# Kernel tuning notes

Measured on AMD Instinct MI355X. Metric: run time of the kernel, lower is better.

## Reference

```python
import jax, jax.numpy as jnp
import numpy as np

B, C, K, T = 8, 256, 64, 1000
NORM_EPS = 1e-12


def setup_inputs() -> dict:
    key = jax.random.key(0)
    k_x, k_codes, k_scales = jax.random.split(key, 3)
    init_val = 1.0 / (K * C) ** 0.5
    x = jax.random.normal(k_x, (B, C, T), dtype=jnp.float32)
    codes = jax.random.uniform(k_codes, (C, K), dtype=jnp.float32,
                               minval=-init_val, maxval=init_val)
    scales = jax.random.uniform(k_scales, (K,), dtype=jnp.float32,
                                minval=0.0, maxval=1.0)
    return {"x": x, "codes": codes, "scales": scales}


def l2_normalize(t, axis, eps=NORM_EPS):
    n = jnp.sqrt(jnp.sum(t * t, axis=axis, keepdims=True))
    n = jnp.maximum(n, eps)
    return t / n


def reference(x, codes, scales):
    # x: (B, C, T); codes: (C, K); scales: (K,)
    residual = x[:, :, None, :] - codes[None, :, :, None]      # (B, C, K, T)
    residual_l2sqr = jnp.sum(residual * residual, axis=1)      # (B, K, T)
    weights_tc = jax.nn.softmax(-scales[None, :, None] * residual_l2sqr, axis=1)  # softmax over codes K
    embeddings = jnp.einsum('bckt,bkt->bkc', residual, weights_tc) / x.shape[-1]  # (B, K, C)
    embeddings = l2_normalize(embeddings, axis=-1)
    return embeddings
```

## Files before the change

### kernel.cpp

```cpp
#include <hip/hip_runtime.h>

constexpr int Bn  = 8;
constexpr int Cn  = 256;
constexpr int Kn  = 64;
constexpr int Tn  = 1000;
constexpr int CH  = 32;
constexpr int NCH = 32;

__global__ __launch_bounds__(512) void lde_ab(
    const float* __restrict__ x,
    const float* __restrict__ codes,
    const float* __restrict__ scales,
    float* __restrict__ part,
    float* __restrict__ Sp)
{
    __shared__ float xs[Cn * 33];
    __shared__ float cds[Cn * 64];
    __shared__ float ws[Kn * 36];
    __shared__ float xsq[CH];
    __shared__ float cpw[8 * 64];
    __shared__ float spw[8 * 64];

    const int tid  = threadIdx.x;
    const int wave = tid >> 6;
    const int lane = tid & 63;
    const int b    = blockIdx.x >> 5;
    const int ch   = blockIdx.x & 31;
    const int t0   = ch * CH;

    {
        const float4* cg = (const float4*)codes;
        float4*       cd = (float4*)cds;
#pragma unroll
        for (int r = 0; r < 8; ++r) cd[r * 512 + tid] = cg[r * 512 + tid];
    }

    {
        const float* xb = x + (size_t)b * Cn * Tn;
#pragma unroll
        for (int r = 0; r < 4; ++r) {
            int idx = r * 512 + tid;
            int c = idx >> 3, q = idx & 7;
            int t = t0 + 4 * q;
            float4 v;
            if (t + 3 < Tn) {
                v = *(const float4*)(xb + c * Tn + t);
            } else {
                v.x = (t     < Tn) ? xb[c * Tn + t]     : 0.f;
                v.y = (t + 1 < Tn) ? xb[c * Tn + t + 1] : 0.f;
                v.z = (t + 2 < Tn) ? xb[c * Tn + t + 2] : 0.f;
                v.w = (t + 3 < Tn) ? xb[c * Tn + t + 3] : 0.f;
            }
            float* d = xs + c * 33 + 4 * q;
            d[0] = v.x; d[1] = v.y; d[2] = v.z; d[3] = v.w;
        }
    }
    __syncthreads();

    {
        float cs = 0.f;
#pragma unroll 8
        for (int j = 0; j < 32; ++j) {
            float v = cds[(wave * 32 + j) * 64 + lane];
            cs = fmaf(v, v, cs);
        }
        cpw[wave * 64 + lane] = cs;
    }

    {
        const int kp    = lane >> 5;
        const int t     = lane & 31;
        const int kbase = wave * 8 + kp * 4;
        float m0 = 0.f, m1 = 0.f, m2 = 0.f, m3 = 0.f, xa = 0.f;
#pragma unroll 4
        for (int c = 0; c < Cn; ++c) {
            float4 cv = *(const float4*)(cds + c * 64 + kbase);
            float  xv = xs[c * 33 + t];
            m0 = fmaf(cv.x, xv, m0);
            m1 = fmaf(cv.y, xv, m1);
            m2 = fmaf(cv.z, xv, m2);
            m3 = fmaf(cv.w, xv, m3);
            xa = fmaf(xv, xv, xa);
        }
        ws[(kbase + 0) * 36 + t] = m0;
        ws[(kbase + 1) * 36 + t] = m1;
        ws[(kbase + 2) * 36 + t] = m2;
        ws[(kbase + 3) * 36 + t] = m3;
        if (tid < 32) xsq[tid] = xa;
    }
    __syncthreads();

    {
        const float sc  = scales[lane];
        float csq = 0.f;
#pragma unroll
        for (int w = 0; w < 8; ++w) csq += cpw[w * 64 + lane];
        float sp = 0.f;
#pragma unroll
        for (int j = 0; j < 4; ++j) {
            int t = wave * 4 + j;
            float mkt   = ws[lane * 36 + t];
            float logit = -sc * (xsq[t] - 2.f * mkt + csq);
            float mx = logit;
#pragma unroll
            for (int off = 32; off >= 1; off >>= 1)
                mx = fmaxf(mx, __shfl_xor(mx, off, 64));
            float e = __expf(logit - mx);
            float s = e;
#pragma unroll
            for (int off = 32; off >= 1; off >>= 1)
                s += __shfl_xor(s, off, 64);
            float wv = e * __builtin_amdgcn_rcpf(s);
            if (t0 + t >= Tn) wv = 0.f;
            sp += wv;
            ws[lane * 36 + t] = wv;
        }
        spw[wave * 64 + lane] = sp;
    }
    __syncthreads();

    if (wave == 0) {
        float s8 = 0.f;
#pragma unroll
        for (int w = 0; w < 8; ++w) s8 += spw[w * 64 + lane];
        Sp[((size_t)b * Kn + lane) * NCH + ch] = s8;
    }

    {
        const int k0 = wave * 8;
        float acc[4][8];
#pragma unroll
        for (int cc = 0; cc < 4; ++cc)
#pragma unroll
            for (int kk = 0; kk < 8; ++kk) acc[cc][kk] = 0.f;

#pragma unroll 2
        for (int q = 0; q < 8; ++q) {
            float xv[4][4];
#pragma unroll
            for (int cc = 0; cc < 4; ++cc) {
                const float* xp = xs + (lane + 64 * cc) * 33 + 4 * q;
                xv[cc][0] = xp[0]; xv[cc][1] = xp[1];
                xv[cc][2] = xp[2]; xv[cc][3] = xp[3];
            }
#pragma unroll
            for (int kk = 0; kk < 8; ++kk) {
                float4 wq = *(const float4*)(ws + (k0 + kk) * 36 + 4 * q);
#pragma unroll
                for (int cc = 0; cc < 4; ++cc) {
                    float a = acc[cc][kk];
                    a = fmaf(xv[cc][0], wq.x, a);
                    a = fmaf(xv[cc][1], wq.y, a);
                    a = fmaf(xv[cc][2], wq.z, a);
                    a = fmaf(xv[cc][3], wq.w, a);
                    acc[cc][kk] = a;
                }
            }
        }

#pragma unroll
        for (int kk = 0; kk < 8; ++kk) {
            float* pb = part + (((size_t)b * Kn + k0 + kk) * NCH + ch) * Cn + lane;
#pragma unroll
            for (int cc = 0; cc < 4; ++cc)
                pb[64 * cc] = acc[cc][kk];
        }
    }
}

__global__ __launch_bounds__(256) void lde_finish(
    const float* __restrict__ part,
    const float* __restrict__ Sp,
    const float* __restrict__ codes,
    float* __restrict__ out)
{
    const int b    = blockIdx.x >> 6;
    const int k    = blockIdx.x & 63;
    const int tid  = threadIdx.x;
    const int lane = tid & 63;
    const int wave = tid >> 6;

    __shared__ float red[4];

    float s = Sp[((size_t)b * Kn + k) * NCH + (tid & 31)];
#pragma unroll
    for (int off = 16; off >= 1; off >>= 1) s += __shfl_xor(s, off, 64);

    const int c = tid;
    const float* pb = part + ((size_t)b * Kn + k) * NCH * Cn + c;
    float val = 0.f;
#pragma unroll
    for (int chk = 0; chk < NCH; ++chk) val += pb[chk * Cn];

    float e = (val - codes[c * Kn + k] * s) * (1.0f / (float)Tn);

    float q = e * e;
#pragma unroll
    for (int off = 32; off >= 1; off >>= 1) q += __shfl_xor(q, off, 64);
    if (lane == 0) red[wave] = q;
    __syncthreads();
    float n = sqrtf(red[0] + red[1] + red[2] + red[3]);

    out[((size_t)b * Kn + k) * Cn + c] = e * __builtin_amdgcn_rcpf(fmaxf(n, 1e-12f));
}

extern "C" void kernel_launch(void* const* d_in, const int* in_sizes, int n_in,
                              void* d_out, int out_size, void* d_ws, size_t ws_size,
                              hipStream_t stream) {
    const float* x      = (const float*)d_in[0];
    const float* codes  = (const float*)d_in[1];
    const float* scales = (const float*)d_in[2];
    float* out = (float*)d_out;

    float* part = (float*)d_ws;
    float* Sp   = (float*)d_ws + (size_t)Bn * Kn * NCH * Cn;

    lde_ab    <<<Bn * NCH, 512, 0, stream>>>(x, codes, scales, part, Sp);
    lde_finish<<<Bn * Kn,  256, 0, stream>>>(part, Sp, codes, out);
}
```

Measured before the change: 84.03 us.

## Use bf16 MFMA for both GEMMs and precompute transposed bf16 codes

Both matmuls in the main kernel (codes·x for the logits and weights·x for the partial embeddings) now use 16x16x32 bf16 MFMA instructions instead of scalar FP32 FMAs. Inputs and softmax weights are converted to bf16 in shared memory. A new prep kernel transposes the codes to bf16 and computes their squared norms once, so each block no longer loads the full fp32 codebook into shared memory. The changes shrink shared memory per block and the FMA work, at the cost of an extra launch and reduced precision in both matmuls.

```diff
diff --git a/kernel.cpp b/kernel.cpp
--- a/kernel.cpp
+++ b/kernel.cpp
@@ -1,4 +1,5 @@
 #include <hip/hip_runtime.h>
+#include <stdint.h>
 
 constexpr int Bn  = 8;
 constexpr int Cn  = 256;
@@ -7,18 +8,54 @@
 constexpr int CH  = 32;
 constexpr int NCH = 32;
 
+constexpr int XC_P = 40;
+constexpr int XT_P = 264;
+constexpr int WA_P = 40;
+constexpr int MW_P = 36;
+
+typedef float f32x4 __attribute__((ext_vector_type(4)));
+typedef __bf16 bf16x8 __attribute__((ext_vector_type(8)));
+
+__device__ __forceinline__ unsigned short f2bf(float f) {
+    unsigned u = __float_as_uint(f);
+    return (unsigned short)((u + 0x7FFFu + ((u >> 16) & 1u)) >> 16);
+}
+
+__global__ __launch_bounds__(256) void lde_prep(
+    const float* __restrict__ codes, unsigned short* __restrict__ cT,
+    float* __restrict__ csq)
+{
+    const int k = blockIdx.x, c = threadIdx.x;
+    const int lane = c & 63, wv = c >> 6;
+    float v = codes[c * Kn + k];
+    cT[k * Cn + c] = f2bf(v);
+    float q = v * v;
+#pragma unroll
+    for (int off = 32; off >= 1; off >>= 1) q += __shfl_xor(q, off, 64);
+    __shared__ float red[4];
+    if (lane == 0) red[wv] = q;
+    __syncthreads();
+    if (c == 0) csq[k] = red[0] + red[1] + red[2] + red[3];
+}
+
+union SmemU {
+    unsigned short xT[CH * XT_P];
+    unsigned short wa[Kn * WA_P];
+};
+
 __global__ __launch_bounds__(512) void lde_ab(
     const float* __restrict__ x,
-    const float* __restrict__ codes,
+    const unsigned short* __restrict__ cT,
+    const float* __restrict__ csq_g,
     const float* __restrict__ scales,
     float* __restrict__ part,
     float* __restrict__ Sp)
 {
-    __shared__ float xs[Cn * 33];
-    __shared__ float cds[Cn * 64];
-    __shared__ float ws[Kn * 36];
+    __shared__ __align__(16) unsigned short xc[Cn * XC_P];
+    __shared__ __align__(16) SmemU u;
+    __shared__ float Mw[Kn * MW_P];
+    __shared__ float xsqp[16 * 33];
     __shared__ float xsq[CH];
-    __shared__ float cpw[8 * 64];
     __shared__ float spw[8 * 64];
 
     const int tid  = threadIdx.x;
@@ -27,80 +64,90 @@
     const int b    = blockIdx.x >> 5;
     const int ch   = blockIdx.x & 31;
     const int t0   = ch * CH;
-
-    {
-        const float4* cg = (const float4*)codes;
-        float4*       cd = (float4*)cds;
-#pragma unroll
-        for (int r = 0; r < 8; ++r) cd[r * 512 + tid] = cg[r * 512 + tid];
-    }
-
-    {
-        const float* xb = x + (size_t)b * Cn * Tn;
-#pragma unroll
-        for (int r = 0; r < 4; ++r) {
-            int idx = r * 512 + tid;
-            int c = idx >> 3, q = idx & 7;
-            int t = t0 + 4 * q;
-            float4 v;
-            if (t + 3 < Tn) {
-                v = *(const float4*)(xb + c * Tn + t);
-            } else {
-                v.x = (t     < Tn) ? xb[c * Tn + t]     : 0.f;
-                v.y = (t + 1 < Tn) ? xb[c * Tn + t + 1] : 0.f;
-                v.z = (t + 2 < Tn) ? xb[c * Tn + t + 2] : 0.f;
-                v.w = (t + 3 < Tn) ? xb[c * Tn + t + 3] : 0.f;
+    const int n    = lane & 15;
+    const int q    = lane >> 4;
+    const float* xb = x + (size_t)b * Cn * Tn;
+
+#pragma unroll
+    for (int r = 0; r < 4; ++r) {
+        int idx = r * 512 + tid;
+        int c = idx >> 3, qq = idx & 7;
+        int t = t0 + 4 * qq;
+        float4 v;
+        if (t + 3 < Tn) {
+            v = *(const float4*)(xb + c * Tn + t);
+        } else {
+            v.x = (t     < Tn) ? xb[c * Tn + t]     : 0.f;
+            v.y = (t + 1 < Tn) ? xb[c * Tn + t + 1] : 0.f;
+            v.z = (t + 2 < Tn) ? xb[c * Tn + t + 2] : 0.f;
+            v.w = (t + 3 < Tn) ? xb[c * Tn + t + 3] : 0.f;
+        }
+        *(ushort4*)(xc + c * XC_P + 4 * qq) =
+            make_ushort4(f2bf(v.x), f2bf(v.y), f2bf(v.z), f2bf(v.w));
+    }
+
+    {
+        int tl = tid & 31, s = tid >> 5;
+        float a = 0.f;
+        if (t0 + tl < Tn) {
+            const float* xp = xb + (s * 16) * Tn + t0 + tl;
+#pragma unroll
+            for (int i = 0; i < 16; ++i) {
+                float v = xp[i * Tn];
+                a = fmaf(v, v, a);
             }
-            float* d = xs + c * 33 + 4 * q;
-            d[0] = v.x; d[1] = v.y; d[2] = v.z; d[3] = v.w;
-        }
-    }
-    __syncthreads();
-
-    {
-        float cs = 0.f;
-#pragma unroll 8
-        for (int j = 0; j < 32; ++j) {
-            float v = cds[(wave * 32 + j) * 64 + lane];
-            cs = fmaf(v, v, cs);
-        }
-        cpw[wave * 64 + lane] = cs;
-    }
-
-    {
-        const int kp    = lane >> 5;
-        const int t     = lane & 31;
-        const int kbase = wave * 8 + kp * 4;
-        float m0 = 0.f, m1 = 0.f, m2 = 0.f, m3 = 0.f, xa = 0.f;
-#pragma unroll 4
-        for (int c = 0; c < Cn; ++c) {
-            float4 cv = *(const float4*)(cds + c * 64 + kbase);
-            float  xv = xs[c * 33 + t];
-            m0 = fmaf(cv.x, xv, m0);
-            m1 = fmaf(cv.y, xv, m1);
-            m2 = fmaf(cv.z, xv, m2);
-            m3 = fmaf(cv.w, xv, m3);
-            xa = fmaf(xv, xv, xa);
-        }
-        ws[(kbase + 0) * 36 + t] = m0;
-        ws[(kbase + 1) * 36 + t] = m1;
-        ws[(kbase + 2) * 36 + t] = m2;
-        ws[(kbase + 3) * 36 + t] = m3;
-        if (tid < 32) xsq[tid] = xa;
-    }
-    __syncthreads();
-
-    {
-        const float sc  = scales[lane];
-        float csq = 0.f;
-#pragma unroll
-        for (int w = 0; w < 8; ++w) csq += cpw[w * 64 + lane];
+        }
+        xsqp[s * 33 + tl] = a;
+    }
+    __syncthreads();
+
+#pragma unroll
+    for (int r = 0; r < 2; ++r) {
+        int idx = r * 512 + tid;
+        int t = idx & 31, cg = idx >> 5;
+        unsigned short tmp[8];
+#pragma unroll
+        for (int i = 0; i < 8; ++i) tmp[i] = xc[(cg * 8 + i) * XC_P + t];
+        *(ushort4*)(u.xT + t * XT_P + cg * 8)     = make_ushort4(tmp[0], tmp[1], tmp[2], tmp[3]);
+        *(ushort4*)(u.xT + t * XT_P + cg * 8 + 4) = make_ushort4(tmp[4], tmp[5], tmp[6], tmp[7]);
+    }
+    if (tid < CH) {
+        float a = 0.f;
+#pragma unroll
+        for (int s = 0; s < 16; ++s) a += xsqp[s * 33 + tid];
+        xsq[tid] = a;
+    }
+    __syncthreads();
+
+    {
+        const int kt = wave & 3, tt = wave >> 2;
+        const int k = kt * 16 + n;
+        const int t = tt * 16 + n;
+        f32x4 acc = {0.f, 0.f, 0.f, 0.f};
+        const unsigned short* Ab = cT + k * Cn + q * 8;
+        const unsigned short* Bb = u.xT + t * XT_P + q * 8;
+#pragma unroll
+        for (int c0 = 0; c0 < Cn; c0 += 32) {
+            bf16x8 aF = *(const bf16x8*)(Ab + c0);
+            bf16x8 bF = *(const bf16x8*)(Bb + c0);
+            acc = __builtin_amdgcn_mfma_f32_16x16x32_bf16(aF, bF, acc, 0, 0, 0);
+        }
+#pragma unroll
+        for (int r = 0; r < 4; ++r)
+            Mw[(kt * 16 + q * 4 + r) * MW_P + tt * 16 + n] = acc[r];
+    }
+    __syncthreads();
+
+    {
+        const float sc = scales[lane];
+        const float cq = csq_g[lane];
+        unsigned short wh[4];
         float sp = 0.f;
 #pragma unroll
         for (int j = 0; j < 4; ++j) {
             int t = wave * 4 + j;
-            float mkt   = ws[lane * 36 + t];
-            float logit = -sc * (xsq[t] - 2.f * mkt + csq);
+            float m     = Mw[lane * MW_P + t];
+            float logit = -sc * (xsq[t] - 2.f * m + cq);
             float mx = logit;
 #pragma unroll
             for (int off = 32; off >= 1; off >>= 1)
@@ -110,11 +157,13 @@
 #pragma unroll
             for (int off = 32; off >= 1; off >>= 1)
                 s += __shfl_xor(s, off, 64);
-            float wv = e * __builtin_amdgcn_rcpf(s);
+            float wv = e / s;
             if (t0 + t >= Tn) wv = 0.f;
             sp += wv;
-            ws[lane * 36 + t] = wv;
-        }
+            wh[j] = f2bf(wv);
+        }
+        *(ushort4*)(u.wa + lane * WA_P + wave * 4) =
+            make_ushort4(wh[0], wh[1], wh[2], wh[3]);
         spw[wave * 64 + lane] = sp;
     }
     __syncthreads();
@@ -125,45 +174,19 @@
         for (int w = 0; w < 8; ++w) s8 += spw[w * 64 + lane];
         Sp[((size_t)b * Kn + lane) * NCH + ch] = s8;
     }
-
-    {
-        const int k0 = wave * 8;
-        float acc[4][8];
-#pragma unroll
-        for (int cc = 0; cc < 4; ++cc)
-#pragma unroll
-            for (int kk = 0; kk < 8; ++kk) acc[cc][kk] = 0.f;
-
-#pragma unroll 2
-        for (int q = 0; q < 8; ++q) {
-            float xv[4][4];
-#pragma unroll
-            for (int cc = 0; cc < 4; ++cc) {
-                const float* xp = xs + (lane + 64 * cc) * 33 + 4 * q;
-                xv[cc][0] = xp[0]; xv[cc][1] = xp[1];
-                xv[cc][2] = xp[2]; xv[cc][3] = xp[3];
-            }
-#pragma unroll
-            for (int kk = 0; kk < 8; ++kk) {
-                float4 wq = *(const float4*)(ws + (k0 + kk) * 36 + 4 * q);
-#pragma unroll
-                for (int cc = 0; cc < 4; ++cc) {
-                    float a = acc[cc][kk];
-                    a = fmaf(xv[cc][0], wq.x, a);
-                    a = fmaf(xv[cc][1], wq.y, a);
-                    a = fmaf(xv[cc][2], wq.z, a);
-                    a = fmaf(xv[cc][3], wq.w, a);
-                    acc[cc][kk] = a;
-                }
-            }
-        }
-
-#pragma unroll
-        for (int kk = 0; kk < 8; ++kk) {
-            float* pb = part + (((size_t)b * Kn + k0 + kk) * NCH + ch) * Cn + lane;
-#pragma unroll
-            for (int cc = 0; cc < 4; ++cc)
-                pb[64 * cc] = acc[cc][kk];
+    {
+        const int kt = wave & 3, hf = wave >> 2;
+        bf16x8 aF = *(const bf16x8*)(u.wa + (kt * 16 + n) * WA_P + q * 8);
+#pragma unroll
+        for (int i = 0; i < 8; ++i) {
+            int c0 = (hf * 8 + i) * 16;
+            bf16x8 bF = *(const bf16x8*)(xc + (c0 + n) * XC_P + q * 8);
+            f32x4 acc = {0.f, 0.f, 0.f, 0.f};
+            acc = __builtin_amdgcn_mfma_f32_16x16x32_bf16(aF, bF, acc, 0, 0, 0);
+            float* pb = part + ((size_t)(b * Kn + kt * 16 + q * 4) * NCH + ch) * Cn + c0 + n;
+#pragma unroll
+            for (int r = 0; r < 4; ++r)
+                pb[(size_t)r * NCH * Cn] = acc[r];
         }
     }
 }
@@ -194,14 +217,14 @@
 
     float e = (val - codes[c * Kn + k] * s) * (1.0f / (float)Tn);
 
-    float q = e * e;
-#pragma unroll
-    for (int off = 32; off >= 1; off >>= 1) q += __shfl_xor(q, off, 64);
-    if (lane == 0) red[wave] = q;
-    __syncthreads();
-    float n = sqrtf(red[0] + red[1] + red[2] + red[3]);
-
-    out[((size_t)b * Kn + k) * Cn + c] = e * __builtin_amdgcn_rcpf(fmaxf(n, 1e-12f));
+    float qq = e * e;
+#pragma unroll
+    for (int off = 32; off >= 1; off >>= 1) qq += __shfl_xor(qq, off, 64);
+    if (lane == 0) red[wave] = qq;
+    __syncthreads();
+    float nn = sqrtf(red[0] + red[1] + red[2] + red[3]);
+
+    out[((size_t)b * Kn + k) * Cn + c] = e / fmaxf(nn, 1e-12f);
 }
 
 extern "C" void kernel_launch(void* const* d_in, const int* in_sizes, int n_in,
@@ -213,8 +236,11 @@
     float* out = (float*)d_out;
 
     float* part = (float*)d_ws;
-    float* Sp   = (float*)d_ws + (size_t)Bn * Kn * NCH * Cn;
-
-    lde_ab    <<<Bn * NCH, 512, 0, stream>>>(x, codes, scales, part, Sp);
+    float* Sp   = part + (size_t)Bn * Kn * NCH * Cn;
+    float* csq  = Sp + (size_t)Bn * Kn * NCH;
+    unsigned short* cT = (unsigned short*)(csq + 64);
+
+    lde_prep  <<<Kn,       256, 0, stream>>>(codes, cT, csq);
+    lde_ab    <<<Bn * NCH, 512, 0, stream>>>(x, cT, csq, scales, part, Sp);
     lde_finish<<<Bn * Kn,  256, 0, stream>>>(part, Sp, codes, out);
 }
```

Result: faster. 78.06 us (-7.1%).
